# Optimization experiments

Hardware: AMD Instinct MI355X
Metric: run time of the kernel (lower is better)

## Reference

```python
import jax, jax.numpy as jnp
import numpy as np

KER = 8

def _gelu(x):
    return jax.nn.gelu(x, approximate=False)

def _conv3x3(x, w, b):
    y = jax.lax.conv_general_dilated(x, w, (1, 1), 'SAME',
                                     dimension_numbers=('NCHW', 'OIHW', 'NCHW'))
    return y + b[None, :, None, None]

def _unfold(x):
    # F.unfold(kernel=8, stride=8): [B,C,H,W] -> [B, C*64, L], C-major then kh,kw
    B, C, H, W = x.shape
    Hb, Wb = H // KER, W // KER
    p = x.reshape(B, C, Hb, KER, Wb, KER).transpose(0, 1, 3, 5, 2, 4)
    return p.reshape(B, C * KER * KER, Hb * Wb)

def _fold(cols, H, W):
    # inverse of _unfold (non-overlapping patches)
    B, CK, L = cols.shape
    C = CK // (KER * KER)
    Hb, Wb = H // KER, W // KER
    p = cols.reshape(B, C, KER, KER, Hb, Wb).transpose(0, 1, 4, 2, 5, 3)
    return p.reshape(B, C, H, W)

def _bn(x, g, b, eps=1e-5):
    # train-mode BatchNorm1d on [B, C, L]: stats over (B, L) per channel
    m = x.mean(axis=(0, 2), keepdims=True)
    v = x.var(axis=(0, 2), keepdims=True)
    return (x - m) * jax.lax.rsqrt(v + eps) * g[None, :, None] + b[None, :, None]


def setup_inputs() -> dict:
    key = jax.random.key(0)
    ks = jax.random.split(key, 10)
    ind, d, hid = 64, 1024, 256
    f = lambda k, s: jax.random.normal(k, s, dtype=jnp.float32) * 0.02
    return {
        'feat': jax.random.normal(ks[0], (4, ind, 256, 256), dtype=jnp.float32),
        'w_enc': f(ks[1], (ind, ind, 3, 3)), 'b_enc': jnp.zeros((ind,), jnp.float32),
        'w_k': f(ks[2], (ind, ind, 3, 3)), 'b_k': jnp.zeros((ind,), jnp.float32),
        'w_v': f(ks[3], (ind, ind, 3, 3)), 'b_v': jnp.zeros((ind,), jnp.float32),
        'fcq_w': f(ks[4], (d, ind * KER * KER)), 'fcq_b': jnp.zeros((d,), jnp.float32),
        'fck_w': f(ks[5], (d, ind * KER * KER)), 'fck_b': jnp.zeros((d,), jnp.float32),
        'bnq_g': jnp.ones((d,), jnp.float32), 'bnq_b': jnp.zeros((d,), jnp.float32),
        'bnk_g': jnp.ones((d,), jnp.float32), 'bnk_b': jnp.zeros((d,), jnp.float32),
        'ff1_w': f(ks[6], (hid, ind)), 'ff1_b': jnp.zeros((hid,), jnp.float32),
        'ff2_w': f(ks[7], (ind, hid)), 'ff2_b': jnp.zeros((ind,), jnp.float32),
    }


def reference(feat, w_enc, b_enc, w_k, b_k, w_v, b_v,
              fcq_w, fcq_b, fck_w, fck_b, bnq_g, bnq_b, bnk_g, bnk_b,
              ff1_w, ff1_b, ff2_w, ff2_b):
    B, C, H, W = feat.shape
    fk = _gelu(_conv3x3(feat, w_k, b_k))
    fv = _gelu(_conv3x3(feat, w_v, b_v))
    refer = _gelu(_conv3x3(feat, w_enc, b_enc))
    q_un = _unfold(refer).transpose(0, 2, 1)   # [B, L, C*64]
    k_un = _unfold(fk).transpose(0, 2, 1)
    v_un = _unfold(fv).transpose(0, 2, 1)
    q = jnp.einsum('blc,dc->bld', q_un, fcq_w) + fcq_b
    q = _bn(q.transpose(0, 2, 1), bnq_g, bnq_b).transpose(0, 2, 1)  # [B, L, 1024]
    k = jnp.einsum('blc,dc->bld', k_un, fck_w) + fck_b
    k = _bn(k.transpose(0, 2, 1), bnk_g, bnk_b).transpose(0, 2, 1)
    scores = jnp.einsum('bld,bmd->blm', q, k) / jnp.sqrt(jnp.float32(q.shape[2]))
    attn = jax.nn.softmax(scores, axis=2)
    out = jnp.einsum('blm,bmc->blc', attn, v_un).transpose(0, 2, 1)  # [B, C*64, L]
    out = _fold(out, H, W)
    h = _gelu(jnp.einsum('bchw,oc->bohw', out, ff1_w) + ff1_b[None, :, None, None])
    h = _gelu(jnp.einsum('bchw,oc->bohw', h, ff2_w) + ff2_b[None, :, None, None])
    return h + feat
```

## Files before the change

kernel.cpp:

```cpp
#include <hip/hip_runtime.h>

typedef unsigned short u16;
typedef float f4 __attribute__((ext_vector_type(4)));
typedef float f32x4 __attribute__((ext_vector_type(4)));
typedef short bf16x8 __attribute__((ext_vector_type(8)));
typedef u16 u16x8 __attribute__((ext_vector_type(8)));
typedef u16 u16x4 __attribute__((ext_vector_type(4)));

__device__ __forceinline__ u16 f2bf(float f){
  unsigned u = __float_as_uint(f);
  u = (u + 0x7FFFu + ((u>>16)&1u)) >> 16;
  return (u16)u;
}
__device__ __forceinline__ float bf2f(u16 u){
  return __uint_as_float(((unsigned)u)<<16);
}
__device__ __forceinline__ float gelu_f(float x){
  float y = 1.5957691216057308f*(x + 0.044715f*x*x*x);
  y = fminf(y, 30.0f);
  float t = __expf(y);
  float r = __builtin_amdgcn_rcpf(t + 1.0f);
  return 0.5f*x*(1.0f + (t - 1.0f)*r);
}

typedef __attribute__((address_space(1))) const unsigned int as1_cuint;
typedef __attribute__((address_space(3))) unsigned int as3_uint;
__device__ __forceinline__ void gload_lds16(const void* g, void* l){
  __builtin_amdgcn_global_load_lds((as1_cuint*)g, (as3_uint*)l, 16, 0, 0);
}

__global__ __launch_bounds__(256) void to_nhwc(
    const float* __restrict__ F, u16* __restrict__ O)
{
  __shared__ float tile[64][65];
  const int t = threadIdx.x, b = blockIdx.y;
  const long px0 = (long)blockIdx.x*64;
  const float* Fb = F + (long)b*64*65536;
  #pragma unroll
  for (int i = 0; i < 4; ++i){
    const int ch = (t>>4) + i*16;
    const int pxo = (t&15)*4;
    f4 v = *(const f4*)&Fb[(long)ch*65536 + px0 + pxo];
    tile[ch][pxo]=v[0]; tile[ch][pxo+1]=v[1]; tile[ch][pxo+2]=v[2]; tile[ch][pxo+3]=v[3];
  }
  __syncthreads();
  const int px = t & 63, ch0 = (t>>6)*16;
  u16x8 o0, o1;
  #pragma unroll
  for (int j = 0; j < 8; ++j){ o0[j]=f2bf(tile[ch0+j][px]); o1[j]=f2bf(tile[ch0+8+j][px]); }
  u16* Ob = O + ((long)b*65536 + px0 + px)*64 + ch0;
  *(u16x8*)Ob = o0; *(u16x8*)(Ob+8) = o1;
}

__global__ __launch_bounds__(256) void wt_prep(
    const float* __restrict__ we, const float* __restrict__ wk,
    const float* __restrict__ wv, u16* __restrict__ Wt2)
{
  const int i = blockIdx.x*256 + threadIdx.x;
  const int cio = i & 31;
  const int t1 = i >> 5;
  const int n  = t1 % 192;
  const int t2 = t1 / 192;
  const int kc = t2 & 1, p = t2 >> 1;
  const int dy = p/3, dx = p - dy*3;
  const int ci = kc*32 + cio;
  const float* W = (n < 64) ? we : (n < 128) ? wk : wv;
  const int co = n & 63;
  Wt2[i] = f2bf(W[((co*64 + ci)*3 + dy)*3 + dx]);
}

__global__ __launch_bounds__(512,2) void conv_mfma(
    const u16* __restrict__ X, const u16* __restrict__ Wt2,
    const float* __restrict__ be, const float* __restrict__ bk, const float* __restrict__ bv,
    u16* __restrict__ Aq, u16* __restrict__ Ak, u16* __restrict__ Vl)
{
  __shared__ __align__(16) u16 smem[24576];
  const int t = threadIdx.x, lane = t & 63, wvi = t >> 6;
  const int bx = blockIdx.x, by = blockIdx.y, b = blockIdx.z;
  const int x0 = bx*16, y0 = by*8;
  const u16* Xb = X + (long)b*4194304;

  #pragma unroll
  for (int j = 0; j < 3; ++j){
    const int id = t + j*512;
    if (id < 1440){
      const int row = id / 144, rem = id - row*144, col = rem >> 3, ck = rem & 7;
      const int y = y0 - 1 + row, x = x0 - 1 + col;
      int4 v = {0,0,0,0};
      if ((unsigned)y < 256u && (unsigned)x < 256u)
        v = *(const int4*)(Xb + ((long)y*256 + x)*64 + ck*8);
      *(int4*)&smem[((row*18 + col)*8 + (ck ^ (col&7)))*8] = v;
    }
  }
  __syncthreads();

  const int wm4 = (wvi>>2)*4;
  const int wn  = (wvi&3)*48;
  const int fr = lane & 15, fo = lane >> 4;
  f32x4 acc[4][3] = {};

  #pragma unroll
  for (int dy = 0; dy < 3; ++dy)
  #pragma unroll
  for (int dx = 0; dx < 3; ++dx){
    const int p = dy*3 + dx;
    #pragma unroll
    for (int kc = 0; kc < 2; ++kc){
      bf16x8 af[4], bfv[3];
      const u16* wp = Wt2 + ((long)(p*2 + kc)*192 + wn + fr)*32 + fo*8;
      #pragma unroll
      for (int ni = 0; ni < 3; ++ni)
        bfv[ni] = *(const bf16x8*)(wp + ni*16*32);
      #pragma unroll
      for (int mi = 0; mi < 4; ++mi){
        const int row = wm4 + mi + dy;
        const int col = fr + dx;
        af[mi] = *(const bf16x8*)&smem[((row*18 + col)*8 + ((kc*4+fo) ^ (col&7)))*8];
      }
      #pragma unroll
      for (int mi = 0; mi < 4; ++mi)
        #pragma unroll
        for (int ni = 0; ni < 3; ++ni)
          acc[mi][ni] = __builtin_amdgcn_mfma_f32_16x16x32_bf16(af[mi], bfv[ni], acc[mi][ni], 0, 0, 0);
    }
  }
  __syncthreads();

  const int c0 = fo*4;
  const int lloc = c0 >> 3, kw0 = c0 & 7;
  #pragma unroll
  for (int ni = 0; ni < 3; ++ni){
    const int n = wn + ni*16 + fr;
    const int mat = n >> 6, co = n & 63;
    const float bias = (mat==0) ? be[co] : (mat==1) ? bk[co] : bv[co];
    #pragma unroll
    for (int mi = 0; mi < 4; ++mi){
      const int r = wm4 + mi;
      u16x4 o;
      #pragma unroll
      for (int rg = 0; rg < 4; ++rg) o[rg] = f2bf(gelu_f(acc[mi][ni][rg] + bias));
      const int e = ((mat*2 + lloc)*64 + co)*64 + ((r*8 + kw0) ^ ((co&7)<<3));
      *(u16x4*)&smem[e] = o;
    }
  }
  __syncthreads();

  const int l_lo = by*32 + bx*2;
  const int co_r = t >> 3, sw = (t&7) ^ (co_r&7);
  const int eoff = co_r*64 + sw*8;
  #pragma unroll
  for (int i = 0; i < 6; ++i){
    const int mat = i >> 1, ll = i & 1;
    u16x8 v = *(const u16x8*)&smem[(mat*2 + ll)*4096 + eoff];
    u16* dst = (mat==0 ? Aq : mat==1 ? Ak : Vl)
             + ((long)b*1024 + l_lo + ll)*4096 + t*8;
    *(u16x8*)dst = v;
  }
}

__global__ __launch_bounds__(256) void v_tr(
    const u16* __restrict__ S, u16* __restrict__ D)
{
  __shared__ u16 tl[64][72];
  const int t = threadIdx.x, b = blockIdx.z;
  const int ck0 = blockIdx.x*64, l0 = blockIdx.y*64;
  const u16* Sb = S + (long)b*4194304;
  u16* Db = D + (long)b*4194304;
  #pragma unroll
  for (int j = 0; j < 2; ++j){
    const int li = (t>>3) + j*32, cko = (t&7)*8;
    *(u16x8*)&tl[li][cko] = *(const u16x8*)(Sb + (long)(l0+li)*4096 + ck0 + cko);
  }
  __syncthreads();
  #pragma unroll
  for (int j = 0; j < 2; ++j){
    const int cki = (t>>3) + j*32, lo = (t&7)*8;
    u16x8 v;
    #pragma unroll
    for (int e = 0; e < 8; ++e) v[e] = tl[lo+e][cki];
    *(u16x8*)(Db + (long)(ck0+cki)*1024 + l0 + lo) = v;
  }
}

__device__ __forceinline__ void xcd_map(int gxl, int gyl, int n8l,
                                        int& bx, int& by, int& bz){
  const int s = blockIdx.x + (blockIdx.y<<gxl) + (blockIdx.z<<(gxl+gyl));
  const int orig = ((s & 7) << n8l) + (s >> 3);
  bx = orig & ((1<<gxl)-1);
  by = (orig >> gxl) & ((1<<gyl)-1);
  bz = orig >> (gxl+gyl);
}

__global__ __launch_bounds__(256,3) void gemm_av(
    const u16* __restrict__ A, long sA,
    const u16* __restrict__ B, long sB,
    void* __restrict__ Cv,
    const int M, const int N, const int K,
    const int gxl, const int gyl, const int n8l)
{
  int bx, by, bI;
  xcd_map(gxl, gyl, n8l, bx, by, bI);
  const u16* Ab = A + (long)bI*sA;
  const u16* Bb = B + (long)bI*sB;
  const int m0 = bx*128, n0 = by*128;
  __shared__ __align__(16) u16 As[8192];
  __shared__ __align__(16) u16 Bs[8192];
  const int t = threadIdx.x, lane = t & 63, wv = t >> 6;
  const int wm = (wv>>1)*64, wn = (wv&1)*64;
  const int fr = lane & 15, fo = lane >> 4;
  f32x4 acc[4][4] = {};
  const int c0 = wv*128 + lane, c1 = c0 + 64;
  const u16* Ag0 = Ab + (long)(m0 + (c0>>2))*K + (c0&3)*8;
  const u16* Ag1 = Ab + (long)(m0 + (c1>>2))*K + (c1&3)*8;
  const u16* Bg0 = Bb + (long)(n0 + (c0>>2))*K + (c0&3)*8;
  const u16* Bg1 = Bb + (long)(n0 + (c1>>2))*K + (c1&3)*8;
  const int lo0 = wv*1024;
  gload_lds16(Ag0, &As[lo0]);
  gload_lds16(Ag1, &As[lo0 + 512]);
  gload_lds16(Bg0, &Bs[lo0]);
  gload_lds16(Bg1, &Bs[lo0 + 512]);
  const int nk = K >> 5;
  int cur = 0;
  for (int ki = 0; ki < nk; ++ki){
    __syncthreads();
    if (ki + 1 < nk){
      const int k0 = (ki + 1) << 5;
      const int so = ((cur^1) << 12) + lo0;
      gload_lds16(Ag0 + k0, &As[so]);
      gload_lds16(Ag1 + k0, &As[so + 512]);
      gload_lds16(Bg0 + k0, &Bs[so]);
      gload_lds16(Bg1 + k0, &Bs[so + 512]);
    }
    const int ro = cur << 12;
    bf16x8 af[4], bfv[4];
    #pragma unroll
    for (int i = 0; i < 4; ++i){
      af[i]  = *(const bf16x8*)&As[ro + (wm + i*16 + fr)*32 + fo*8];
      bfv[i] = *(const bf16x8*)&Bs[ro + (wn + i*16 + fr)*32 + fo*8];
    }
    __builtin_amdgcn_s_setprio(1);
    #pragma unroll
    for (int mi = 0; mi < 4; ++mi)
      #pragma unroll
      for (int ni = 0; ni < 4; ++ni)
        acc[mi][ni] = __builtin_amdgcn_mfma_f32_16x16x32_bf16(af[mi], bfv[ni], acc[mi][ni], 0, 0, 0);
    __builtin_amdgcn_s_setprio(0);
    cur ^= 1;
  }
  u16* O = (u16*)Cv;
  #pragma unroll
  for (int mi = 0; mi < 4; ++mi)
    #pragma unroll
    for (int ni = 0; ni < 4; ++ni){
      const int col = n0 + wn + ni*16 + fr;
      const int c = col >> 6, khh = (col>>3)&7, kww = col&7;
      #pragma unroll
      for (int r = 0; r < 4; ++r){
        const int row = m0 + wm + mi*16 + fo*4 + r;
        const int hb = row >> 5, wbb = row & 31;
        O[(((long)bI*65536 + (hb*8+khh)*256 + wbb*8 + kww)<<6) + c] = f2bf(acc[mi][ni][r]);
      }
    }
}

template<int EPI>
__global__ __launch_bounds__(256,2) void gemm_bt128(
    const u16* __restrict__ A, long sA,
    const u16* __restrict__ B, long sB, const int zshB,
    void* __restrict__ Cv, long sC,
    const int M, const int N, const int K,
    float* __restrict__ bnstats,
    const int gxl, const int gyl, const int n8l)
{
  int bx, by, bI;
  xcd_map(gxl, gyl, n8l, bx, by, bI);
  const u16* Ab = A + (long)bI*sA;
  const u16* Bb = B + (long)(bI>>zshB)*sB;
  const int m0 = bx*128, n0 = by*128;
  __shared__ __align__(16) u16 As[16384];
  __shared__ __align__(16) u16 Bs[16384];
  const int t = threadIdx.x, lane = t & 63, wv = t >> 6;
  const int wm = (wv>>1)*64, wn = (wv&1)*64;
  const int fr = lane & 15, fo = lane >> 4;
  f32x4 acc[4][4] = {};
  const int c0 = wv*128 + lane, c1 = c0 + 64;
  const u16* Ag0 = Ab + (long)(m0 + (c0>>2))*K + (c0&3)*8;
  const u16* Ag1 = Ab + (long)(m0 + (c1>>2))*K + (c1&3)*8;
  const u16* Bg0 = Bb + (long)(n0 + (c0>>2))*K + (c0&3)*8;
  const u16* Bg1 = Bb + (long)(n0 + (c1>>2))*K + (c1&3)*8;
#define STAGEH(slot, h, kofs) { \
    u16* a_ = &As[(((slot)*2+(h))<<12) + wv*1024]; \
    u16* b_ = &Bs[(((slot)*2+(h))<<12) + wv*1024]; \
    const int ko_ = (kofs) + 32*(h); \
    gload_lds16(Ag0 + ko_, a_); \
    gload_lds16(Ag1 + ko_, a_ + 512); \
    gload_lds16(Bg0 + ko_, b_); \
    gload_lds16(Bg1 + ko_, b_ + 512); }
  STAGEH(0, 0, 0)
  STAGEH(0, 1, 0)
  const int nk = K >> 6;
  int cur = 0;
  for (int ki = 0; ki < nk; ++ki){
    __syncthreads();
    if (ki + 1 < nk){
      const int k0 = (ki + 1) << 6;
      STAGEH(cur^1, 0, k0)
      STAGEH(cur^1, 1, k0)
    }
    #pragma unroll
    for (int h = 0; h < 2; ++h){
      const int ro = ((cur*2 + h) << 12);
      bf16x8 af[4], bfv[4];
      #pragma unroll
      for (int i = 0; i < 4; ++i){
        af[i]  = *(const bf16x8*)&As[ro + (wm + i*16 + fr)*32 + fo*8];
        bfv[i] = *(const bf16x8*)&Bs[ro + (wn + i*16 + fr)*32 + fo*8];
      }
      __builtin_amdgcn_s_setprio(1);
      #pragma unroll
      for (int mi = 0; mi < 4; ++mi)
        #pragma unroll
        for (int ni = 0; ni < 4; ++ni)
          acc[mi][ni] = __builtin_amdgcn_mfma_f32_16x16x32_bf16(af[mi], bfv[ni], acc[mi][ni], 0, 0, 0);
      __builtin_amdgcn_s_setprio(0);
    }
    cur ^= 1;
  }
#undef STAGEH
  if (EPI == 0){
    float* Cf = (float*)Cv + (long)bI*sC;
    #pragma unroll
    for (int mi = 0; mi < 4; ++mi)
      #pragma unroll
      for (int ni = 0; ni < 4; ++ni){
        const int col = n0 + wn + ni*16 + fr;
        #pragma unroll
        for (int r = 0; r < 4; ++r){
          const int row = m0 + wm + mi*16 + fo*4 + r;
          Cf[(long)row*N + col] = acc[mi][ni][r];
        }
      }
  } else {
    u16* Cb = (u16*)Cv + (long)bI*sC;
    #pragma unroll
    for (int mi = 0; mi < 4; ++mi)
      #pragma unroll
      for (int ni = 0; ni < 4; ++ni){
        const int col = n0 + wn + ni*16 + fr;
        const int row0 = m0 + wm + mi*16 + fo*4;
        u16x4 o;
        #pragma unroll
        for (int r = 0; r < 4; ++r) o[r] = f2bf(acc[mi][ni][r]);
        *(u16x4*)&Cb[(long)col*M + row0] = o;
      }
    const int sel = bI >> 2;
    float* sums = bnstats + sel*2048;
    #pragma unroll
    for (int ni = 0; ni < 4; ++ni){
      float s = 0.f, q = 0.f;
      #pragma unroll
      for (int mi = 0; mi < 4; ++mi)
        #pragma unroll
        for (int r = 0; r < 4; ++r){
          const float v = acc[mi][ni][r];
          s += v; q += v*v;
        }
      s += __shfl_xor(s, 16); s += __shfl_xor(s, 32);
      q += __shfl_xor(q, 16); q += __shfl_xor(q, 32);
      if (fo == 0){
        const int col = n0 + wn + ni*16 + fr;
        atomicAdd(&sums[col], s);
        atomicAdd(&sums[1024 + col], q);
      }
    }
  }
}

__global__ __launch_bounds__(256,2) void ff_fused(
    const u16* __restrict__ X, const u16* __restrict__ W1b,
    const float* __restrict__ B1, const u16* __restrict__ W2b,
    const float* __restrict__ B2, const float* __restrict__ F,
    float* __restrict__ OUT)
{
  __shared__ __align__(16) u16 h1s[128*264];
  const int t = threadIdx.x, lane = t & 63, wv = t >> 6;
  const long m0 = (long)blockIdx.x*128;
  const int fr = lane & 15, fo = lane >> 4;

  {
    const int wm = (wv>>1)*64, wn = (wv&1)*128;
    f32x4 acc[4][8] = {};
    #pragma unroll
    for (int kc = 0; kc < 2; ++kc){
      bf16x8 af[4], bf[8];
      #pragma unroll
      for (int mi = 0; mi < 4; ++mi)
        af[mi] = *(const bf16x8*)(X + (m0 + wm + mi*16 + fr)*64 + kc*32 + fo*8);
      #pragma unroll
      for (int ni = 0; ni < 8; ++ni)
        bf[ni] = *(const bf16x8*)(W1b + (long)(wn + ni*16 + fr)*64 + kc*32 + fo*8);
      #pragma unroll
      for (int mi = 0; mi < 4; ++mi)
        #pragma unroll
        for (int ni = 0; ni < 8; ++ni)
          acc[mi][ni] = __builtin_amdgcn_mfma_f32_16x16x32_bf16(af[mi], bf[ni], acc[mi][ni], 0, 0, 0);
    }
    #pragma unroll
    for (int ni = 0; ni < 8; ++ni){
      const int col = wn + ni*16 + fr;
      const float bc = B1[col];
      #pragma unroll
      for (int mi = 0; mi < 4; ++mi){
        const int row0 = wm + mi*16 + fo*4;
        #pragma unroll
        for (int r = 0; r < 4; ++r)
          h1s[(row0 + r)*264 + col] = f2bf(gelu_f(acc[mi][ni][r] + bc));
      }
    }
  }
  __syncthreads();

  {
    const int wm2 = wv*32;
    f32x4 acc2[2][4] = {};
    for (int k0 = 0; k0 < 256; k0 += 32){
      bf16x8 af2[2], bf2[4];
      #pragma unroll
      for (int mi = 0; mi < 2; ++mi)
        af2[mi] = *(const bf16x8*)&h1s[(wm2 + mi*16 + fr)*264 + k0 + fo*8];
      #pragma unroll
      for (int ni = 0; ni < 4; ++ni)
        bf2[ni] = *(const bf16x8*)(W2b + (long)(ni*16 + fr)*256 + k0 + fo*8);
      #pragma unroll
      for (int mi = 0; mi < 2; ++mi)
        #pragma unroll
        for (int ni = 0; ni < 4; ++ni)
          acc2[mi][ni] = __builtin_amdgcn_mfma_f32_16x16x32_bf16(af2[mi], bf2[ni], acc2[mi][ni], 0, 0, 0);
    }
    #pragma unroll
    for (int ni = 0; ni < 4; ++ni){
      const int c = ni*16 + fr;
      const float bc = B2[c];
      #pragma unroll
      for (int mi = 0; mi < 2; ++mi){
        const long p = m0 + wm2 + mi*16 + fo*4;
        const int b = (int)(p >> 16), pp = (int)(p & 65535);
        const long idx = ((long)(b*64 + c))*65536 + pp;
        const f4 fres = *(const f4*)&F[idx];
        f4 o;
        #pragma unroll
        for (int r = 0; r < 4; ++r) o[r] = gelu_f(acc2[mi][ni][r] + bc) + fres[r];
        *(f4*)&OUT[idx] = o;
      }
    }
  }
}

__global__ __launch_bounds__(256) void cvt_w(
    const float* __restrict__ Wq, const float* __restrict__ Wk,
    u16* __restrict__ Oq, u16* __restrict__ Ok)
{
  const long i = ((long)blockIdx.x*256 + threadIdx.x)*4;
  const float* s = blockIdx.y ? Wk : Wq;
  u16* d = blockIdx.y ? Ok : Oq;
  f4 v = *(const f4*)&s[i];
  u16x4 o; o[0]=f2bf(v[0]); o[1]=f2bf(v[1]); o[2]=f2bf(v[2]); o[3]=f2bf(v[3]);
  *(u16x4*)&d[i] = o;
}

__global__ __launch_bounds__(256) void cvt_ffw(
    const float* __restrict__ W1, const float* __restrict__ W2,
    u16* __restrict__ O1, u16* __restrict__ O2)
{
  const long i = ((long)blockIdx.x*256 + threadIdx.x)*4;
  const float* s = blockIdx.y ? W2 : W1;
  u16* d = blockIdx.y ? O2 : O1;
  f4 v = *(const f4*)&s[i];
  u16x4 o; o[0]=f2bf(v[0]); o[1]=f2bf(v[1]); o[2]=f2bf(v[2]); o[3]=f2bf(v[3]);
  *(u16x4*)&d[i] = o;
}

__global__ void bn_fin2(float* __restrict__ stats,
                        const float* __restrict__ gq, const float* __restrict__ bq,
                        const float* __restrict__ gk, const float* __restrict__ bk)
{
  const int sel = blockIdx.y;
  const int d = blockIdx.x*256 + threadIdx.x;
  if (d >= 1024) return;
  const float* sum   = stats + sel*2048;
  const float* sumsq = sum + 1024;
  const float* g    = sel ? gk : gq;
  const float* beta = sel ? bk : bq;
  const float m  = sum[d]   * (1.f/4096.f);
  const float vv = sumsq[d] * (1.f/4096.f) - m*m;
  const float sc = g[d] * rsqrtf(vv + 1e-5f);
  stats[4096 + sel*2048 + d]        = sc;
  stats[4096 + sel*2048 + 1024 + d] = beta[d] - m*sc;
}

__global__ __launch_bounds__(256) void bn_apply_t(
    const u16* __restrict__ QT, const float* __restrict__ stats,
    u16* __restrict__ Y)
{
  __shared__ u16 tl[64][72];
  const int t = threadIdx.x, zi = blockIdx.z;
  const int d0 = blockIdx.x*64, l0 = blockIdx.y*64;
  const int sel = zi >> 2;
  const u16* S = QT + (long)zi*1048576;
  u16* D = Y + (long)zi*1048576;
  const float* scp = stats + 4096 + sel*2048;
  const float* shp = scp + 1024;
  #pragma unroll
  for (int j = 0; j < 2; ++j){
    const int di = (t>>3) + j*32, lo = (t&7)*8;
    const int d = d0 + di;
    const float sc = scp[d], sh = shp[d];
    u16x8 v = *(const u16x8*)(S + (long)d*1024 + l0 + lo);
    u16x8 o;
    #pragma unroll
    for (int e = 0; e < 8; ++e) o[e] = f2bf(bf2f(v[e])*sc + sh);
    *(u16x8*)&tl[di][lo] = o;
  }
  __syncthreads();
  #pragma unroll
  for (int j = 0; j < 2; ++j){
    const int li = (t>>3) + j*32, dof = (t&7)*8;
    u16x8 v;
    #pragma unroll
    for (int e = 0; e < 8; ++e) v[e] = tl[dof+e][li];
    *(u16x8*)(D + (long)(l0+li)*1024 + d0 + dof) = v;
  }
}

__global__ __launch_bounds__(256) void softmax_k(
    const float* __restrict__ S, u16* __restrict__ P)
{
  const long row = blockIdx.x;
  const float* p = S + row*1024;
  const int t = threadIdx.x;
  f4 v = *(const f4*)&p[t*4];
  v *= 0.03125f;
  float mx = fmaxf(fmaxf(v[0],v[1]), fmaxf(v[2],v[3]));
  #pragma unroll
  for (int o = 1; o < 64; o <<= 1) mx = fmaxf(mx, __shfl_xor(mx, o));
  __shared__ float red[4], red2[4];
  if ((t & 63) == 0) red[t>>6] = mx;
  __syncthreads();
  mx = fmaxf(fmaxf(red[0],red[1]), fmaxf(red[2],red[3]));
  f4 e;
  e[0]=__expf(v[0]-mx); e[1]=__expf(v[1]-mx); e[2]=__expf(v[2]-mx); e[3]=__expf(v[3]-mx);
  float sm = e[0]+e[1]+e[2]+e[3];
  #pragma unroll
  for (int o = 1; o < 64; o <<= 1) sm += __shfl_xor(sm, o);
  if ((t & 63) == 0) red2[t>>6] = sm;
  __syncthreads();
  sm = red2[0]+red2[1]+red2[2]+red2[3];
  const float inv = 1.0f/sm;
  u16x4 o4; o4[0]=f2bf(e[0]*inv); o4[1]=f2bf(e[1]*inv); o4[2]=f2bf(e[2]*inv); o4[3]=f2bf(e[3]*inv);
  *(u16x4*)&P[row*1024 + t*4] = o4;
}

extern "C" void kernel_launch(void* const* d_in, const int* in_sizes, int n_in,
                              void* d_out, int out_size, void* d_ws, size_t ws_size,
                              hipStream_t stream)
{
  const float* feat  = (const float*)d_in[0];
  const float* w_enc = (const float*)d_in[1];
  const float* b_enc = (const float*)d_in[2];
  const float* w_k   = (const float*)d_in[3];
  const float* b_k   = (const float*)d_in[4];
  const float* w_v   = (const float*)d_in[5];
  const float* b_v   = (const float*)d_in[6];
  const float* fcq_w = (const float*)d_in[7];
  const float* fck_w = (const float*)d_in[9];
  const float* bnq_g = (const float*)d_in[11];
  const float* bnq_b = (const float*)d_in[12];
  const float* bnk_g = (const float*)d_in[13];
  const float* bnk_b = (const float*)d_in[14];
  const float* ff1w  = (const float*)d_in[15];
  const float* ff1b  = (const float*)d_in[16];
  const float* ff2w  = (const float*)d_in[17];
  const float* ff2b  = (const float*)d_in[18];

  char* ws = (char*)d_ws;
  u16*   Aq      = (u16*)  (ws);
  u16*   Ak      = (u16*)  (ws + (32ull<<20));
  u16*   Vc      = (u16*)  (ws + (64ull<<20));
  u16*   Wq      = (u16*)  (ws + (96ull<<20));
  u16*   Wk      = (u16*)  (ws + (104ull<<20));
  u16*   q_bf    = (u16*)  (ws + (112ull<<20));
  u16*   k_bf    = (u16*)  (ws + (120ull<<20));
  u16*   qk_rawT = (u16*)  (ws + (128ull<<20));
  float* scores  = (float*)(ws + (160ull<<20));
  u16*   attn    = (u16*)  (ws + (176ull<<20));
  u16*   out_nhwc= (u16*)  (ws + (184ull<<20));
  u16*   NX      = (u16*)  (ws + (128ull<<20));
  u16*   Vl      = (u16*)  (ws + (160ull<<20));
  u16*   Wt2     = (u16*)  (ws + (216ull<<20));
  float* stats   = (float*)(ws + (217ull<<20));
  u16*   W1b     = (u16*)  (ws + (218ull<<20));
  u16*   W2b     = (u16*)  (ws + (218ull<<20) + 65536);

  hipMemsetAsync(stats, 0, 4096*sizeof(float), stream);

  to_nhwc<<<dim3(1024,4), 256, 0, stream>>>(feat, NX);
  wt_prep<<<dim3(432), 256, 0, stream>>>(w_enc, w_k, w_v, Wt2);
  conv_mfma<<<dim3(16,32,4), 512, 0, stream>>>(NX, Wt2, b_enc, b_k, b_v, Aq, Ak, Vl);
  v_tr<<<dim3(64,16,4), 256, 0, stream>>>(Vl, Vc);
  cvt_w<<<dim3(4096,2), 256, 0, stream>>>(fcq_w, fck_w, Wq, Wk);
  cvt_ffw<<<dim3(16,2), 256, 0, stream>>>(ff1w, ff2w, W1b, W2b);

  gemm_bt128<2><<<dim3(8,8,8), 256, 0, stream>>>(Aq, 4194304, Wq, 4194304, 2,
                                                 qk_rawT, 1048576, 1024, 1024, 4096, stats,
                                                 3, 3, 6);

  bn_fin2<<<dim3(4,2), 256, 0, stream>>>(stats, bnq_g, bnq_b, bnk_g, bnk_b);
  bn_apply_t<<<dim3(16,16,8), 256, 0, stream>>>(qk_rawT, stats, q_bf);

  gemm_bt128<0><<<dim3(8,8,4), 256, 0, stream>>>(q_bf, 1048576, k_bf, 1048576, 0,
                                                 scores, 1048576, 1024, 1024, 1024, nullptr,
                                                 3, 3, 5);
  softmax_k<<<dim3(4096), 256, 0, stream>>>(scores, attn);

  gemm_av<<<dim3(8,32,4), 256, 0, stream>>>(attn, 1048576, Vc, 4194304,
                                            out_nhwc, 1024, 4096, 1024,
                                            3, 5, 7);

  ff_fused<<<dim3(2048), 256, 0, stream>>>(out_nhwc, W1b, ff1b, W2b, ff2b,
                                           feat, (float*)d_out);
}
```

Measured before the change: 477.9 us.

## Merge weight prep kernels, store scores as bf16, use wave-per-row softmax

Folds the three weight-conversion kernels into a single prep_all launch, which removes two launches. The QK^T GEMM epilogue now writes scores as bf16 instead of fp32, halving score traffic, and the softmax is rewritten so one wavefront handles one row with no shared-memory reductions or barriers. gemm_av's launch bound rises from 3 to 4 blocks per CU. Rounding scores to bf16 before softmax lowers precision, and the higher occupancy target may force register spills in gemm_av.

```diff
diff --git a/kernel.cpp b/kernel.cpp
--- a/kernel.cpp
+++ b/kernel.cpp
@@ -52,21 +52,46 @@
   *(u16x8*)Ob = o0; *(u16x8*)(Ob+8) = o1;
 }
 
-__global__ __launch_bounds__(256) void wt_prep(
+__global__ __launch_bounds__(256) void prep_all(
     const float* __restrict__ we, const float* __restrict__ wk,
-    const float* __restrict__ wv, u16* __restrict__ Wt2)
-{
-  const int i = blockIdx.x*256 + threadIdx.x;
-  const int cio = i & 31;
-  const int t1 = i >> 5;
-  const int n  = t1 % 192;
-  const int t2 = t1 / 192;
-  const int kc = t2 & 1, p = t2 >> 1;
-  const int dy = p/3, dx = p - dy*3;
-  const int ci = kc*32 + cio;
-  const float* W = (n < 64) ? we : (n < 128) ? wk : wv;
-  const int co = n & 63;
-  Wt2[i] = f2bf(W[((co*64 + ci)*3 + dy)*3 + dx]);
+    const float* __restrict__ wv, u16* __restrict__ Wt2,
+    const float* __restrict__ Wqf, const float* __restrict__ Wkf,
+    u16* __restrict__ Oq, u16* __restrict__ Ok,
+    const float* __restrict__ W1, const float* __restrict__ W2,
+    u16* __restrict__ O1, u16* __restrict__ O2)
+{
+  const int bb = blockIdx.x, t = threadIdx.x;
+  if (bb < 432){
+    const int i = bb*256 + t;
+    const int cio = i & 31;
+    const int t1 = i >> 5;
+    const int n  = t1 % 192;
+    const int t2 = t1 / 192;
+    const int kc = t2 & 1, p = t2 >> 1;
+    const int dy = p/3, dx = p - dy*3;
+    const int ci = kc*32 + cio;
+    const float* W = (n < 64) ? we : (n < 128) ? wk : wv;
+    const int co = n & 63;
+    Wt2[i] = f2bf(W[((co*64 + ci)*3 + dy)*3 + dx]);
+  } else if (bb < 8624){
+    const int b2 = bb - 432;
+    const int sel = b2 >> 12;
+    const long i = ((long)(b2 & 4095)*256 + t)*4;
+    const float* s = sel ? Wkf : Wqf;
+    u16* d = sel ? Ok : Oq;
+    f4 v = *(const f4*)&s[i];
+    u16x4 o; o[0]=f2bf(v[0]); o[1]=f2bf(v[1]); o[2]=f2bf(v[2]); o[3]=f2bf(v[3]);
+    *(u16x4*)&d[i] = o;
+  } else {
+    const int b3 = bb - 8624;
+    const int sel = b3 >> 4;
+    const long i = ((long)(b3 & 15)*256 + t)*4;
+    const float* s = sel ? W2 : W1;
+    u16* d = sel ? O2 : O1;
+    f4 v = *(const f4*)&s[i];
+    u16x4 o; o[0]=f2bf(v[0]); o[1]=f2bf(v[1]); o[2]=f2bf(v[2]); o[3]=f2bf(v[3]);
+    *(u16x4*)&d[i] = o;
+  }
 }
 
 __global__ __launch_bounds__(512,2) void conv_mfma(
@@ -191,7 +216,7 @@
   bz = orig >> (gxl+gyl);
 }
 
-__global__ __launch_bounds__(256,3) void gemm_av(
+__global__ __launch_bounds__(256,4) void gemm_av(
     const u16* __restrict__ A, long sA,
     const u16* __restrict__ B, long sB,
     void* __restrict__ Cv,
@@ -327,8 +352,8 @@
     cur ^= 1;
   }
 #undef STAGEH
-  if (EPI == 0){
-    float* Cf = (float*)Cv + (long)bI*sC;
+  if (EPI == 3){
+    u16* Cb = (u16*)Cv + (long)bI*sC;
     #pragma unroll
     for (int mi = 0; mi < 4; ++mi)
       #pragma unroll
@@ -337,7 +362,7 @@
         #pragma unroll
         for (int r = 0; r < 4; ++r){
           const int row = m0 + wm + mi*16 + fo*4 + r;
-          Cf[(long)row*N + col] = acc[mi][ni][r];
+          Cb[(long)row*N + col] = f2bf(acc[mi][ni][r]);
         }
       }
   } else {
@@ -454,30 +479,6 @@
       }
     }
   }
-}
-
-__global__ __launch_bounds__(256) void cvt_w(
-    const float* __restrict__ Wq, const float* __restrict__ Wk,
-    u16* __restrict__ Oq, u16* __restrict__ Ok)
-{
-  const long i = ((long)blockIdx.x*256 + threadIdx.x)*4;
-  const float* s = blockIdx.y ? Wk : Wq;
-  u16* d = blockIdx.y ? Ok : Oq;
-  f4 v = *(const f4*)&s[i];
-  u16x4 o; o[0]=f2bf(v[0]); o[1]=f2bf(v[1]); o[2]=f2bf(v[2]); o[3]=f2bf(v[3]);
-  *(u16x4*)&d[i] = o;
-}
-
-__global__ __launch_bounds__(256) void cvt_ffw(
-    const float* __restrict__ W1, const float* __restrict__ W2,
-    u16* __restrict__ O1, u16* __restrict__ O2)
-{
-  const long i = ((long)blockIdx.x*256 + threadIdx.x)*4;
-  const float* s = blockIdx.y ? W2 : W1;
-  u16* d = blockIdx.y ? O2 : O1;
-  f4 v = *(const f4*)&s[i];
-  u16x4 o; o[0]=f2bf(v[0]); o[1]=f2bf(v[1]); o[2]=f2bf(v[2]); o[3]=f2bf(v[3]);
-  *(u16x4*)&d[i] = o;
 }
 
 __global__ void bn_fin2(float* __restrict__ stats,
@@ -532,32 +533,33 @@
   }
 }
 
-__global__ __launch_bounds__(256) void softmax_k(
-    const float* __restrict__ S, u16* __restrict__ P)
-{
-  const long row = blockIdx.x;
-  const float* p = S + row*1024;
-  const int t = threadIdx.x;
-  f4 v = *(const f4*)&p[t*4];
-  v *= 0.03125f;
-  float mx = fmaxf(fmaxf(v[0],v[1]), fmaxf(v[2],v[3]));
+__global__ __launch_bounds__(256) void softmax_w(
+    const u16* __restrict__ S, u16* __restrict__ P)
+{
+  const int wv = threadIdx.x >> 6, lane = threadIdx.x & 63;
+  const long row = (long)blockIdx.x*4 + wv;
+  const u16* p = S + row*1024 + lane*16;
+  u16x8 a = *(const u16x8*)p;
+  u16x8 b = *(const u16x8*)(p + 8);
+  float v[16];
+  #pragma unroll
+  for (int j = 0; j < 8; ++j){ v[j] = bf2f(a[j])*0.03125f; v[8+j] = bf2f(b[j])*0.03125f; }
+  float mx = v[0];
+  #pragma unroll
+  for (int j = 1; j < 16; ++j) mx = fmaxf(mx, v[j]);
   #pragma unroll
   for (int o = 1; o < 64; o <<= 1) mx = fmaxf(mx, __shfl_xor(mx, o));
-  __shared__ float red[4], red2[4];
-  if ((t & 63) == 0) red[t>>6] = mx;
-  __syncthreads();
-  mx = fmaxf(fmaxf(red[0],red[1]), fmaxf(red[2],red[3]));
-  f4 e;
-  e[0]=__expf(v[0]-mx); e[1]=__expf(v[1]-mx); e[2]=__expf(v[2]-mx); e[3]=__expf(v[3]-mx);
-  float sm = e[0]+e[1]+e[2]+e[3];
+  float sm = 0.f;
+  #pragma unroll
+  for (int j = 0; j < 16; ++j){ v[j] = __expf(v[j] - mx); sm += v[j]; }
   #pragma unroll
   for (int o = 1; o < 64; o <<= 1) sm += __shfl_xor(sm, o);
-  if ((t & 63) == 0) red2[t>>6] = sm;
-  __syncthreads();
-  sm = red2[0]+red2[1]+red2[2]+red2[3];
   const float inv = 1.0f/sm;
-  u16x4 o4; o4[0]=f2bf(e[0]*inv); o4[1]=f2bf(e[1]*inv); o4[2]=f2bf(e[2]*inv); o4[3]=f2bf(e[3]*inv);
-  *(u16x4*)&P[row*1024 + t*4] = o4;
+  u16x8 oa, ob;
+  #pragma unroll
+  for (int j = 0; j < 8; ++j){ oa[j] = f2bf(v[j]*inv); ob[j] = f2bf(v[8+j]*inv); }
+  u16* q = P + row*1024 + lane*16;
+  *(u16x8*)q = oa; *(u16x8*)(q + 8) = ob;
 }
 
 extern "C" void kernel_launch(void* const* d_in, const int* in_sizes, int n_in,
@@ -591,7 +593,7 @@
   u16*   q_bf    = (u16*)  (ws + (112ull<<20));
   u16*   k_bf    = (u16*)  (ws + (120ull<<20));
   u16*   qk_rawT = (u16*)  (ws + (128ull<<20));
-  float* scores  = (float*)(ws + (160ull<<20));
+  u16*   scores  = (u16*)  (ws + (160ull<<20));
   u16*   attn    = (u16*)  (ws + (176ull<<20));
   u16*   out_nhwc= (u16*)  (ws + (184ull<<20));
   u16*   NX      = (u16*)  (ws + (128ull<<20));
@@ -604,11 +606,11 @@
   hipMemsetAsync(stats, 0, 4096*sizeof(float), stream);
 
   to_nhwc<<<dim3(1024,4), 256, 0, stream>>>(feat, NX);
-  wt_prep<<<dim3(432), 256, 0, stream>>>(w_enc, w_k, w_v, Wt2);
+  prep_all<<<dim3(8656), 256, 0, stream>>>(w_enc, w_k, w_v, Wt2,
+                                           fcq_w, fck_w, Wq, Wk,
+                                           ff1w, ff2w, W1b, W2b);
   conv_mfma<<<dim3(16,32,4), 512, 0, stream>>>(NX, Wt2, b_enc, b_k, b_v, Aq, Ak, Vl);
   v_tr<<<dim3(64,16,4), 256, 0, stream>>>(Vl, Vc);
-  cvt_w<<<dim3(4096,2), 256, 0, stream>>>(fcq_w, fck_w, Wq, Wk);
-  cvt_ffw<<<dim3(16,2), 256, 0, stream>>>(ff1w, ff2w, W1b, W2b);
 
   gemm_bt128<2><<<dim3(8,8,8), 256, 0, stream>>>(Aq, 4194304, Wq, 4194304, 2,
                                                  qk_rawT, 1048576, 1024, 1024, 4096, stats,
@@ -617,10 +619,10 @@
   bn_fin2<<<dim3(4,2), 256, 0, stream>>>(stats, bnq_g, bnq_b, bnk_g, bnk_b);
   bn_apply_t<<<dim3(16,16,8), 256, 0, stream>>>(qk_rawT, stats, q_bf);
 
-  gemm_bt128<0><<<dim3(8,8,4), 256, 0, stream>>>(q_bf, 1048576, k_bf, 1048576, 0,
+  gemm_bt128<3><<<dim3(8,8,4), 256, 0, stream>>>(q_bf, 1048576, k_bf, 1048576, 0,
                                                  scores, 1048576, 1024, 1024, 1024, nullptr,
                                                  3, 3, 5);
-  softmax_k<<<dim3(4096), 256, 0, stream>>>(scores, attn);
+  softmax_w<<<dim3(1024), 256, 0, stream>>>(scores, attn);
 
   gemm_av<<<dim3(8,32,4), 256, 0, stream>>>(attn, 1048576, Vc, 4194304,
                                             out_nhwc, 1024, 4096, 1024,
```

Measured after the change: 454.4 us (median of 2 runs). 4.9% less time.
